# Performance work log

Hardware: AMD Instinct MI355X
Metric: run time of the kernel (lower is better)

The kernel has to match this reference:

```python
import jax, jax.numpy as jnp
import numpy as np

# dims
B, L, IN, H, OUT = 2, 2048, 128, 512, 64
NL, ED, N, DR, K = 2, 1024, 16, 32, 4  # n_layers, d_inner=2*H, d_state, dt_rank=ceil(H/16), d_conv


def setup_inputs() -> dict:
    key = jax.random.key(0)
    ks = jax.random.split(key, 18)
    r = lambda k, s: 0.05 * jax.random.normal(k, s, dtype=jnp.float32)
    return {
        "x": jax.random.normal(ks[0], (B, L, IN), dtype=jnp.float32),
        # LiquidNet proj (in_dim -> hidden -> hidden)
        "p_Wi": r(ks[1], (IN, H)), "p_bi": r(ks[2], (H,)), "p_bh": r(ks[3], (H,)),
        "p_Wo": r(ks[4], (H, H)), "p_bo": r(ks[5], (H,)),
        # Mamba layers (stacked over layer axis)
        "m_norm_w": jnp.ones((NL, H), jnp.float32),
        "m_in_W": r(ks[6], (NL, H, 2 * ED)),
        "m_conv_w": r(ks[7], (NL, ED, K)), "m_conv_b": r(ks[8], (NL, ED)),
        "m_xproj_W": r(ks[9], (NL, ED, DR + 2 * N)),
        "m_dt_W": r(ks[10], (NL, DR, ED)), "m_dt_b": r(ks[11], (NL, ED)),
        "m_A_log": jnp.tile(jnp.log(jnp.arange(1, N + 1, dtype=jnp.float32)), (NL, ED, 1)),
        "m_D": jnp.ones((NL, ED), jnp.float32),
        "m_out_W": r(ks[12], (NL, ED, H)),
        # LiquidNet dense (hidden -> out_dim -> out_dim)
        "d_Wi": r(ks[13], (H, OUT)), "d_bi": r(ks[14], (OUT,)), "d_bh": r(ks[15], (OUT,)),
        "d_Wo": r(ks[16], (OUT, OUT)), "d_bo": r(ks[17], (OUT,)),
    }


def _rmsnorm(x, w, eps=1e-5):
    return x * jax.lax.rsqrt(jnp.mean(x * x, axis=-1, keepdims=True) + eps) * w


def _liquid(x, Wi, bi, bh, Wo, bo):
    # liquid cell with zero initial hidden state: h = tanh(i2h(x) + h2h(0))
    h = jnp.tanh(x @ Wi + bi + bh)
    return h @ Wo + bo


def _causal_conv(x, w, b):
    # x: [B, L, ED]; depthwise causal conv with kernel K
    xt = x.transpose(0, 2, 1)  # [B, ED, L]
    y = jax.lax.conv_general_dilated(xt, w[:, None, :], (1,), [(K - 1, 0)],
                                     dimension_numbers=('NCH', 'OIH', 'NCH'),
                                     feature_group_count=ED)
    return (y + b[None, :, None]).transpose(0, 2, 1)


def _ssm(xc, delta, Bm, Cm, A, D):
    # xc/delta: [B,L,ED]; Bm/Cm: [B,L,N]; A: [ED,N]; D: [ED]
    deltaA = jnp.exp(delta[..., None] * A)                              # [B,L,ED,N]
    deltaBx = delta[..., None] * Bm[:, :, None, :] * xc[..., None]      # [B,L,ED,N]

    def step(h, t):
        dA, dBx, Ct = t
        h = dA * h + dBx
        return h, jnp.einsum('bdn,bn->bd', h, Ct)

    h0 = jnp.zeros((xc.shape[0], ED, N), xc.dtype)
    _, ys = jax.lax.scan(step, h0, (deltaA.transpose(1, 0, 2, 3),
                                    deltaBx.transpose(1, 0, 2, 3),
                                    Cm.transpose(1, 0, 2)))
    return ys.transpose(1, 0, 2) + D * xc


def _mamba_block(x, norm_w, in_W, conv_w, conv_b, xproj_W, dt_W, dt_b, A_log, D, out_W):
    xn = _rmsnorm(x, norm_w)
    xz = xn @ in_W                       # [B,L,2*ED]
    xc, z = jnp.split(xz, 2, axis=-1)
    xc = jax.nn.silu(_causal_conv(xc, conv_w, conv_b))
    dbl = xc @ xproj_W                   # [B,L,DR+2N]
    dt, Bm, Cm = dbl[..., :DR], dbl[..., DR:DR + N], dbl[..., DR + N:]
    delta = jax.nn.softplus(dt @ dt_W + dt_b)
    y = _ssm(xc, delta, Bm, Cm, -jnp.exp(A_log), D)
    y = y * jax.nn.silu(z)
    return y @ out_W


def reference(x, p_Wi, p_bi, p_bh, p_Wo, p_bo,
              m_norm_w, m_in_W, m_conv_w, m_conv_b, m_xproj_W, m_dt_W, m_dt_b,
              m_A_log, m_D, m_out_W,
              d_Wi, d_bi, d_bh, d_Wo, d_bo):
    out = _liquid(x, p_Wi, p_bi, p_bh, p_Wo, p_bo)
    for l in range(NL):  # residual Mamba blocks
        out = out + _mamba_block(out, m_norm_w[l], m_in_W[l], m_conv_w[l], m_conv_b[l],
                                 m_xproj_W[l], m_dt_W[l], m_dt_b[l], m_A_log[l], m_D[l], m_out_W[l])
    out = _liquid(out, d_Wi, d_bi, d_bh, d_Wo, d_bo)
    out = out - jnp.tanh(out)  # Tanhshrink
    return out.reshape(-1)
```

## Files before the change

### kernel.cpp

```cpp
#include <hip/hip_runtime.h>
#include <hip/hip_bf16.h>
#include <cstdint>
#include <cstddef>

#define B_   2
#define L_   2048
#define IN_  128
#define H_   512
#define OUT_ 64
#define NL_  2
#define ED_  1024
#define N_   16
#define DR_  32
#define K_   4

static constexpr int M_TOK = B_ * L_;
static constexpr int SEG   = 64;
static constexpr int TS    = L_ / SEG;

typedef __attribute__((ext_vector_type(8))) short bhalf8;
typedef __attribute__((ext_vector_type(4))) float floatx4;

__device__ __forceinline__ ushort bf16bits(float f)
{
    __hip_bfloat16 h = __float2bfloat16(f);
    return *reinterpret_cast<ushort*>(&h);
}

__device__ __forceinline__ void gld_lds16(const ushort* g, ushort* l)
{
    __builtin_amdgcn_global_load_lds(
        (const __attribute__((address_space(1))) unsigned int*)g,
        (__attribute__((address_space(3))) unsigned int*)l, 16, 0, 0);
}

template<int BM, int BN, int BK, int EPI, bool DUAL>
__global__ __launch_bounds__(256)
void mfma_gemm(const ushort* __restrict__ A, int lda,
               const ushort* Bt, int ldb,
               const ushort* Bt2, float* C2,
               const float* __restrict__ b1, const float* __restrict__ b2,
               float* C, __hip_bfloat16* Cb, int ldc,
               int M, int N, int kc)
{
    __shared__ __align__(16) ushort As[BM * BK];
    __shared__ __align__(16) ushort Bs[BN * BK];

    const int tid  = threadIdx.x;
    const int bm   = blockIdx.x * BM, bn = blockIdx.y * BN;
    int kz = 0, kbeg = 0;
    if (DUAL) {
        if (blockIdx.z) { Bt = Bt2; C = C2; }
    } else {
        kz = blockIdx.z; kbeg = kz * kc;
    }
    const int lane = tid & 63, wave = tid >> 6;
    const int wr = wave >> 1, wc = wave & 1;
    constexpr int WM = BM / 2, WN = BN / 2;
    constexpr int FM = WM / 16, FN = WN / 16;
    const int fr = lane & 15, fg = lane >> 4;

    constexpr int ACH = BM * BK / 512;
    constexpr int BCH = BN * BK / 512;
    constexpr int RPC = 512 / BK;
    constexpr int LPR = BK / 8;
    const int sr = lane / LPR;
    const int sc = (lane % LPR) * 8;

    floatx4 acc[FM][FN] = {};

    for (int k0 = kbeg; k0 < kbeg + kc; k0 += BK) {
        #pragma unroll
        for (int i = 0; i < ACH / 4; ++i) {
            const int ci = wave * (ACH / 4) + i;
            const int r  = ci * RPC + sr;
            gld_lds16(&A[(size_t)(bm + r) * lda + k0 + sc], &As[ci * 512]);
        }
        #pragma unroll
        for (int i = 0; i < BCH / 4; ++i) {
            const int ci = wave * (BCH / 4) + i;
            const int r  = ci * RPC + sr;
            gld_lds16(&Bt[(size_t)(bn + r) * ldb + k0 + sc], &Bs[ci * 512]);
        }
        __syncthreads();
        #pragma unroll
        for (int kk = 0; kk < BK; kk += 32) {
            bhalf8 fa[FM], fb[FN];
            #pragma unroll
            for (int m = 0; m < FM; ++m)
                fa[m] = *reinterpret_cast<const bhalf8*>(
                    &As[(wr * WM + m * 16 + fr) * BK + kk + fg * 8]);
            #pragma unroll
            for (int n = 0; n < FN; ++n)
                fb[n] = *reinterpret_cast<const bhalf8*>(
                    &Bs[(wc * WN + n * 16 + fr) * BK + kk + fg * 8]);
            #pragma unroll
            for (int m = 0; m < FM; ++m)
                #pragma unroll
                for (int n = 0; n < FN; ++n)
                    acc[m][n] = __builtin_amdgcn_mfma_f32_16x16x32_bf16(
                        fa[m], fb[n], acc[m][n], 0, 0, 0);
        }
        __syncthreads();
    }

    #pragma unroll
    for (int m = 0; m < FM; ++m) {
        #pragma unroll
        for (int n = 0; n < FN; ++n) {
            const int row0 = bm + wr * WM + m * 16 + fg * 4;
            const int col  = bn + wc * WN + n * 16 + fr;
            #pragma unroll
            for (int r = 0; r < 4; ++r) {
                float v = acc[m][n][r];
                const int row = row0 + r;
                if (EPI == 0) {
                    C[(size_t)row * ldc + col] = v;
                } else if (EPI == 1) {
                    C[(size_t)row * ldc + col] += v;
                } else if (EPI == 2) {
                    Cb[(size_t)row * ldc + col] =
                        __float2bfloat16(tanhf(v + b1[col] + b2[col]));
                } else if (EPI == 3) {
                    C[(size_t)row * ldc + col] = v + b1[col];
                } else if (EPI == 4) {
                    C[(size_t)kz * M * N + (size_t)row * N + col] = v;
                } else if (EPI == 5) {
                    const float w = v + b1[col];
                    C[(size_t)row * ldc + col] = w - tanhf(w);
                } else if (EPI == 6) {
                    const float w = v + b1[col];
                    C[(size_t)row * ldc + col] =
                        fmaxf(w, 0.0f) + log1pf(expf(-fabsf(w)));
                } else if (EPI == 7) {
                    float* cp = C + (size_t)row * ldc + col;
                    const float w = *cp + v;
                    *cp = w;
                    Cb[(size_t)row * ldc + col] = __float2bfloat16(w);
                }
            }
        }
    }
}

template<int NP, int ACT, bool B1, bool B2, int OUTMODE>
__global__ __launch_bounds__(256)
void reduce_part_k(const float* __restrict__ P, const float* __restrict__ b1,
                   const float* __restrict__ b2, float* __restrict__ Of,
                   __hip_bfloat16* __restrict__ Ob, int MN, int Ncols)
{
    const int i = blockIdx.x * 256 + threadIdx.x;
    float s = 0.0f;
    #pragma unroll
    for (int z = 0; z < NP; ++z) s += P[(size_t)z * MN + i];
    const int col = i & (Ncols - 1);
    if (B1) s += b1[col];
    if (B2) s += b2[col];
    if (ACT == 1) s = tanhf(s);
    if (OUTMODE == 0 || OUTMODE == 2) Of[i] = s;
    if (OUTMODE == 1 || OUTMODE == 2) Ob[i] = __float2bfloat16(s);
}

__device__ __forceinline__ void tr32(float (*t)[33],
                                     const float* __restrict__ W,
                                     __hip_bfloat16* __restrict__ Wt,
                                     int K, int N, int local, int gx, int tid)
{
    const int kx = local % gx, ny = local / gx;
    const int k0 = kx * 32, n0 = ny * 32;
    const int c = tid & 31, r4 = tid >> 5;
    #pragma unroll
    for (int i = 0; i < 4; ++i) {
        const int rr = r4 + i * 8;
        t[rr][c] = W[(size_t)(k0 + rr) * N + n0 + c];
    }
    __syncthreads();
    #pragma unroll
    for (int i = 0; i < 4; ++i) {
        const int rr = r4 + i * 8;
        Wt[(size_t)(n0 + rr) * K + k0 + c] = __float2bfloat16(t[c][rr]);
    }
}

__global__ __launch_bounds__(256)
void prep_k(const float* __restrict__ x, __hip_bfloat16* __restrict__ Xb,
            const float* pWi, __hip_bfloat16* TpWi,
            const float* pWo, __hip_bfloat16* TpWo,
            const float* inW, __hip_bfloat16* TinW0, __hip_bfloat16* TinW1,
            const float* xpW, __hip_bfloat16* TxpW0, __hip_bfloat16* TxpW1,
            const float* outW, __hip_bfloat16* ToutW0, __hip_bfloat16* ToutW1,
            const float* dWi, __hip_bfloat16* TdWi,
            const float* dtW, __hip_bfloat16* TdtW0, __hip_bfloat16* TdtW1,
            const float* dWo, __hip_bfloat16* TdWo)
{
    __shared__ float t[32][33];
    const int tid = threadIdx.x;
    int r = blockIdx.x;

    if (r < 512) {
        const int i = (r * 256 + tid) * 4;
        const float4 v = *reinterpret_cast<const float4*>(&x[i]);
        ushort4 u;
        u.x = bf16bits(v.x); u.y = bf16bits(v.y);
        u.z = bf16bits(v.z); u.w = bf16bits(v.w);
        *reinterpret_cast<ushort4*>(&Xb[i]) = u;
        return;
    }
    r -= 512;
    if (r < 64)   { tr32(t, pWi, TpWi, IN_, H_, r, 4, tid); return; }   r -= 64;
    if (r < 256)  { tr32(t, pWo, TpWo, H_, H_, r, 16, tid); return; }   r -= 256;
    if (r < 1024) { tr32(t, inW, TinW0, H_, 2 * ED_, r, 16, tid); return; } r -= 1024;
    if (r < 1024) { tr32(t, inW + (size_t)H_ * 2 * ED_, TinW1, H_, 2 * ED_, r, 16, tid); return; } r -= 1024;
    if (r < 64)   { tr32(t, xpW, TxpW0, ED_, 64, r, 32, tid); return; } r -= 64;
    if (r < 64)   { tr32(t, xpW + (size_t)ED_ * 64, TxpW1, ED_, 64, r, 32, tid); return; } r -= 64;
    if (r < 512)  { tr32(t, outW, ToutW0, ED_, H_, r, 32, tid); return; } r -= 512;
    if (r < 512)  { tr32(t, outW + (size_t)ED_ * H_, ToutW1, ED_, H_, r, 32, tid); return; } r -= 512;
    if (r < 32)   { tr32(t, dWi, TdWi, H_, OUT_, r, 16, tid); return; } r -= 32;
    if (r < 32)   { tr32(t, dtW, TdtW0, DR_, ED_, r, 1, tid); return; } r -= 32;
    if (r < 32)   { tr32(t, dtW + DR_ * ED_, TdtW1, DR_, ED_, r, 1, tid); return; } r -= 32;
    tr32(t, dWo, TdWo, OUT_, OUT_, r, 2, tid);
}
static constexpr int PREP_BLOCKS = 512 + 64 + 256 + 1024 + 1024 + 64 + 64 + 512 + 512 + 32 + 32 + 32 + 4;

__global__ __launch_bounds__(256)
void rmsnorm_k(const float* __restrict__ x, const float* __restrict__ w,
               __hip_bfloat16* __restrict__ o)
{
    const int row = blockIdx.x;
    const int tid = threadIdx.x;
    const float* xr = x + (size_t)row * H_;
    float v0 = xr[tid], v1 = xr[tid + 256];
    float s = v0 * v0 + v1 * v1;
    #pragma unroll
    for (int off = 32; off > 0; off >>= 1) s += __shfl_down(s, off, 64);
    __shared__ float ps[4];
    __shared__ float scale_s;
    const int wave = tid >> 6, lane = tid & 63;
    if (lane == 0) ps[wave] = s;
    __syncthreads();
    if (tid == 0) {
        float tot = ps[0] + ps[1] + ps[2] + ps[3];
        scale_s = rsqrtf(tot * (1.0f / H_) + 1e-5f);
    }
    __syncthreads();
    const float sc = scale_s;
    o[(size_t)row * H_ + tid]       = __float2bfloat16(v0 * sc * w[tid]);
    o[(size_t)row * H_ + tid + 256] = __float2bfloat16(v1 * sc * w[tid + 256]);
}

__global__ __launch_bounds__(256)
void conv_silu_k(const float* __restrict__ xcr, const float* __restrict__ cw,
                 const float* __restrict__ cb, float* __restrict__ xc,
                 __hip_bfloat16* __restrict__ xcb)
{
    const int idx = blockIdx.x * 256 + threadIdx.x;
    const int d4 = (idx & (ED_ / 4 - 1)) * 4;
    const int t  = (idx >> 8) & (L_ - 1);
    const int b  = idx >> 19;
    const size_t base = (size_t)(b * L_ + t) * ED_ + d4;

    float4 x0 = *reinterpret_cast<const float4*>(&xcr[base]);
    float4 x1 = {}, x2 = {}, x3 = {};
    if (t >= 1) x1 = *reinterpret_cast<const float4*>(&xcr[base - 1 * ED_]);
    if (t >= 2) x2 = *reinterpret_cast<const float4*>(&xcr[base - 2 * ED_]);
    if (t >= 3) x3 = *reinterpret_cast<const float4*>(&xcr[base - 3 * ED_]);
    const float4 bias = *reinterpret_cast<const float4*>(&cb[d4]);

    float4 out;
    ushort4 outb;
    #pragma unroll
    for (int j = 0; j < 4; ++j) {
        const float4 w = *reinterpret_cast<const float4*>(&cw[(d4 + j) * 4]);
        float acc = (&bias.x)[j];
        acc += w.w * (&x0.x)[j];
        acc += w.z * (&x1.x)[j];
        acc += w.y * (&x2.x)[j];
        acc += w.x * (&x3.x)[j];
        const float s = acc / (1.0f + __expf(-acc));
        (&out.x)[j] = s;
        (&outb.x)[j] = bf16bits(s);
    }
    *reinterpret_cast<float4*>(&xc[base]) = out;
    *reinterpret_cast<ushort4*>(&xcb[base]) = outb;
}

template<bool P3>
__global__ __launch_bounds__(256)
void ssm_scan_k(const float* __restrict__ delta,
                const float* __restrict__ xc,
                const float* __restrict__ dbl,
                const float* __restrict__ zbuf,
                const float* __restrict__ A_log,
                const float* __restrict__ Dv,
                float* __restrict__ hend, float* __restrict__ pprod,
                const float* __restrict__ hinit,
                __hip_bfloat16* __restrict__ ybuf)
{
    __shared__ float sdl[TS][64];
    __shared__ float sxc[TS][64];
    __shared__ float bc[TS][32];
    const int bx   = blockIdx.x;
    const int seg  = bx & (SEG - 1);
    const int dblk = (bx >> 6) & 15;
    const int b    = bx >> 10;
    const int tid  = threadIdx.x;
    const int dl   = tid >> 2;
    const int ng   = tid & 3;
    const int d    = dblk * 64 + dl;
    const int dbase = dblk * 64;
    const size_t row0 = (size_t)(b * L_ + seg * TS);

    #pragma unroll
    for (int e = 0; e < 8; ++e) {
        const int lin = tid + e * 256;
        sdl[lin >> 6][lin & 63] = delta[(row0 + (lin >> 6)) * ED_ + dbase + (lin & 63)];
    }
    #pragma unroll
    for (int e = 0; e < 8; ++e) {
        const int lin = tid + e * 256;
        sxc[lin >> 6][lin & 63] = xc[(row0 + (lin >> 6)) * ED_ + dbase + (lin & 63)];
    }
    #pragma unroll
    for (int e = 0; e < 4; ++e) {
        const int lin = tid + e * 256;
        bc[lin >> 5][lin & 31] = dbl[(row0 + (lin >> 5)) * 64 + 32 + (lin & 31)];
    }

    float Av[4];
    #pragma unroll
    for (int i = 0; i < 4; ++i) Av[i] = -expf(A_log[d * N_ + ng * 4 + i]);

    float h[4], P[4];
    if (P3) {
        #pragma unroll
        for (int i = 0; i < 4; ++i)
            h[i] = hinit[((size_t)(b * SEG + seg) * N_ + ng * 4 + i) * ED_ + d];
    } else {
        #pragma unroll
        for (int i = 0; i < 4; ++i) { h[i] = 0.0f; P[i] = 1.0f; }
    }
    const float Dd = P3 ? Dv[d] : 0.0f;
    __syncthreads();

    #pragma unroll
    for (int t = 0; t < TS; ++t) {
        const float dvt = sdl[t][dl];
        const float xvt = sxc[t][dl];
        const float dx  = dvt * xvt;
        float ysum = 0.0f;
        #pragma unroll
        for (int i = 0; i < 4; ++i) {
            const float dA = __expf(dvt * Av[i]);
            h[i] = fmaf(dA, h[i], dx * bc[t][ng * 4 + i]);
            if (!P3) P[i] *= dA;
            else     ysum = fmaf(h[i], bc[t][16 + ng * 4 + i], ysum);
        }
        if (P3) {
            float y2 = ysum + __shfl_xor(ysum, 1, 64);
            float y4 = y2 + __shfl_xor(y2, 2, 64);
            if (ng == 0) {
                const float zv = zbuf[(row0 + t) * ED_ + d];
                const float sz = zv / (1.0f + __expf(-zv));
                ybuf[(row0 + t) * ED_ + d] =
                    __float2bfloat16((y4 + Dd * xvt) * sz);
            }
        }
    }

    if (!P3) {
        #pragma unroll
        for (int i = 0; i < 4; ++i) {
            const size_t o = ((size_t)(b * SEG + seg) * N_ + ng * 4 + i) * ED_ + d;
            hend[o]  = h[i];
            pprod[o] = P[i];
        }
    }
}

__global__ __launch_bounds__(256)
void ssm_combine_k(const float* __restrict__ hend, const float* __restrict__ pprod,
                   float* __restrict__ hinit)
{
    const int gid = blockIdx.x * 256 + threadIdx.x;
    const int d = gid & (ED_ - 1);
    const int n = (gid >> 10) & (N_ - 1);
    const int b = gid >> 14;
    size_t o = ((size_t)(b * SEG) * N_ + n) * ED_ + d;
    const size_t stride = (size_t)N_ * ED_;
    float h = 0.0f;
    #pragma unroll 8
    for (int s = 0; s < SEG; ++s) {
        hinit[o] = h;
        h = fmaf(pprod[o], h, hend[o]);
        o += stride;
    }
}

extern "C" void kernel_launch(void* const* d_in, const int* in_sizes, int n_in,
                              void* d_out, int out_size, void* d_ws, size_t ws_size,
                              hipStream_t stream)
{
    const float* x      = (const float*)d_in[0];
    const float* p_Wi   = (const float*)d_in[1];
    const float* p_bi   = (const float*)d_in[2];
    const float* p_bh   = (const float*)d_in[3];
    const float* p_Wo   = (const float*)d_in[4];
    const float* p_bo   = (const float*)d_in[5];
    const float* m_norm = (const float*)d_in[6];
    const float* m_inW  = (const float*)d_in[7];
    const float* m_cw   = (const float*)d_in[8];
    const float* m_cb   = (const float*)d_in[9];
    const float* m_xpW  = (const float*)d_in[10];
    const float* m_dtW  = (const float*)d_in[11];
    const float* m_dtb  = (const float*)d_in[12];
    const float* m_Alog = (const float*)d_in[13];
    const float* m_D    = (const float*)d_in[14];
    const float* m_outW = (const float*)d_in[15];
    const float* d_Wi   = (const float*)d_in[16];
    const float* d_bi   = (const float*)d_in[17];
    const float* d_bh   = (const float*)d_in[18];
    const float* d_Wo   = (const float*)d_in[19];
    const float* d_bo   = (const float*)d_in[20];
    float* out_f = (float*)d_out;
    float* ws = (float*)d_ws;

    float* OUT   = ws;
    float* XCR   = ws + 2097152;
    float* Z     = ws + 6291456;
    float* XC    = ws + 10485760;
    float* DBL   = ws + 14680064;
    float* DELTA = ws + 14942208;
    float* HINIT = ws + 19136512;
    float* BF    = ws + 21233664;
    float* WT    = ws + 23330816;
    float* DBLF  = ws + 25184256;

    float* HEND   = XCR;
    float* PPROD  = XCR + 2097152;
    float* CPARTX = DELTA;
    float* CPART2 = XCR;
    __hip_bfloat16* Xb   = (__hip_bfloat16*)BF;
    __hip_bfloat16* H1b  = (__hip_bfloat16*)(BF + 262144);
    __hip_bfloat16* XNb  = (__hip_bfloat16*)BF;
    __hip_bfloat16* XCb  = (__hip_bfloat16*)BF;
    __hip_bfloat16* YB   = (__hip_bfloat16*)BF;
    __hip_bfloat16* H2b  = (__hip_bfloat16*)BF;
    __hip_bfloat16* OUTb = (__hip_bfloat16*)XC;
    __hip_bfloat16* DBLb = (__hip_bfloat16*)DBLF;

    __hip_bfloat16* WTu     = (__hip_bfloat16*)WT;
    __hip_bfloat16* T_pWi   = WTu;
    __hip_bfloat16* T_pWo   = WTu + 65536;
    __hip_bfloat16* T_inW0  = WTu + 327680;
    __hip_bfloat16* T_inW1  = WTu + 1376256;
    __hip_bfloat16* T_xpW0  = WTu + 2424832;
    __hip_bfloat16* T_xpW1  = WTu + 2490368;
    __hip_bfloat16* T_outW0 = WTu + 2555904;
    __hip_bfloat16* T_outW1 = WTu + 3080192;
    __hip_bfloat16* T_dWi   = WTu + 3604480;
    __hip_bfloat16* T_dtW0  = WTu + 3637248;
    __hip_bfloat16* T_dtW1  = WTu + 3670016;
    __hip_bfloat16* T_dWo   = WTu + 3702784;

    const dim3 blk(256);

    prep_k<<<dim3(PREP_BLOCKS), blk, 0, stream>>>(
        x, Xb, p_Wi, T_pWi, p_Wo, T_pWo, m_inW, T_inW0, T_inW1,
        m_xpW, T_xpW0, T_xpW1, m_outW, T_outW0, T_outW1,
        d_Wi, T_dWi, m_dtW, T_dtW0, T_dtW1, d_Wo, T_dWo);

    mfma_gemm<128, 64, 64, 2, false><<<dim3(32, 8), blk, 0, stream>>>(
        (const ushort*)Xb, IN_, (const ushort*)T_pWi, IN_, nullptr, nullptr,
        p_bi, p_bh, nullptr, H1b, H_, M_TOK, H_, IN_);
    mfma_gemm<128, 64, 64, 3, false><<<dim3(32, 8), blk, 0, stream>>>(
        (const ushort*)H1b, H_, (const ushort*)T_pWo, H_, nullptr, nullptr,
        p_bo, nullptr, OUT, nullptr, H_, M_TOK, H_, H_);

    for (int l = 0; l < NL_; ++l) {
        const float* nw   = m_norm + l * H_;
        const float* cw   = m_cw   + l * ED_ * K_;
        const float* cb   = m_cb   + l * ED_;
        const float* dtb  = m_dtb  + l * ED_;
        const float* Alog = m_Alog + l * ED_ * N_;
        const float* Dv   = m_D    + l * ED_;
        const __hip_bfloat16* TinW  = l ? T_inW1  : T_inW0;
        const __hip_bfloat16* TxpW  = l ? T_xpW1  : T_xpW0;
        const __hip_bfloat16* ToutW = l ? T_outW1 : T_outW0;
        const __hip_bfloat16* TdtW  = l ? T_dtW1  : T_dtW0;

        rmsnorm_k<<<dim3(M_TOK), blk, 0, stream>>>(OUT, nw, XNb);
        mfma_gemm<128, 128, 64, 0, true><<<dim3(32, 8, 2), blk, 0, stream>>>(
            (const ushort*)XNb, H_, (const ushort*)TinW, H_,
            (const ushort*)(TinW + (size_t)ED_ * H_), Z,
            nullptr, nullptr, XCR, nullptr, ED_, M_TOK, ED_, H_);
        conv_silu_k<<<dim3(M_TOK * ED_ / 4 / 256), blk, 0, stream>>>(XCR, cw, cb, XC, XCb);
        mfma_gemm<128, 64, 64, 4, false><<<dim3(32, 1, 8), blk, 0, stream>>>(
            (const ushort*)XCb, ED_, (const ushort*)TxpW, ED_, nullptr, nullptr,
            nullptr, nullptr, CPARTX, nullptr, 64, M_TOK, 64, ED_ / 8);
        reduce_part_k<8, 0, false, false, 2><<<dim3(1024), blk, 0, stream>>>(
            CPARTX, nullptr, nullptr, DBL, DBLb, M_TOK * 64, 64);
        mfma_gemm<128, 64, 32, 6, false><<<dim3(32, 16), blk, 0, stream>>>(
            (const ushort*)DBLb, 64, (const ushort*)TdtW, DR_, nullptr, nullptr,
            dtb, nullptr, DELTA, nullptr, ED_, M_TOK, ED_, DR_);
        ssm_scan_k<false><<<dim3(2048), blk, 0, stream>>>(
            DELTA, XC, DBL, nullptr, Alog, nullptr, HEND, PPROD, nullptr, nullptr);
        ssm_combine_k<<<dim3(128), blk, 0, stream>>>(HEND, PPROD, HINIT);
        ssm_scan_k<true><<<dim3(2048), blk, 0, stream>>>(
            DELTA, XC, DBL, Z, Alog, Dv, nullptr, nullptr, HINIT, YB);
        if (l == 0) {
            mfma_gemm<128, 64, 64, 1, false><<<dim3(32, 8), blk, 0, stream>>>(
                (const ushort*)YB, ED_, (const ushort*)ToutW, ED_, nullptr, nullptr,
                nullptr, nullptr, OUT, nullptr, H_, M_TOK, H_, ED_);
        } else {
            mfma_gemm<128, 64, 64, 7, false><<<dim3(32, 8), blk, 0, stream>>>(
                (const ushort*)YB, ED_, (const ushort*)ToutW, ED_, nullptr, nullptr,
                nullptr, nullptr, OUT, OUTb, H_, M_TOK, H_, ED_);
        }
    }

    mfma_gemm<128, 64, 64, 4, false><<<dim3(32, 1, 8), blk, 0, stream>>>(
        (const ushort*)OUTb, H_, (const ushort*)T_dWi, H_, nullptr, nullptr,
        nullptr, nullptr, CPART2, nullptr, 64, M_TOK, 64, H_ / 8);
    reduce_part_k<8, 1, true, true, 1><<<dim3(1024), blk, 0, stream>>>(
        CPART2, d_bi, d_bh, nullptr, H2b, M_TOK * 64, 64);
    mfma_gemm<128, 64, 64, 5, false><<<dim3(32, 1), blk, 0, stream>>>(
        (const ushort*)H2b, OUT_, (const ushort*)T_dWo, OUT_, nullptr, nullptr,
        d_bo, nullptr, out_f, nullptr, OUT_, M_TOK, OUT_, OUT_);
}
```

Before: 342.5 us.

## Fuse dt projection, softplus and conv recompute into SSM scan kernels

Removes the separate delta GEMM (dt_proj plus softplus) and the fp32 XC buffer. Each scan block now recomputes the causal conv plus SiLU from the raw XCR values and computes delta from dbl and the dt weights in shared memory. This cuts global traffic for the fp32 delta and xc tensors (each written once and read twice) and drops one launch per layer. The cost is redundant FP32 compute in both scan passes and larger shared memory per block, which could lower occupancy.

After: 408.7 us. 19.3% more time.

```diff
diff --git a/kernel.cpp b/kernel.cpp
--- a/kernel.cpp
+++ b/kernel.cpp
@@ -128,10 +128,6 @@
                 } else if (EPI == 5) {
                     const float w = v + b1[col];
                     C[(size_t)row * ldc + col] = w - tanhf(w);
-                } else if (EPI == 6) {
-                    const float w = v + b1[col];
-                    C[(size_t)row * ldc + col] =
-                        fmaxf(w, 0.0f) + log1pf(expf(-fabsf(w)));
                 } else if (EPI == 7) {
                     float* cp = C + (size_t)row * ldc + col;
                     const float w = *cp + v;
@@ -190,7 +186,6 @@
             const float* xpW, __hip_bfloat16* TxpW0, __hip_bfloat16* TxpW1,
             const float* outW, __hip_bfloat16* ToutW0, __hip_bfloat16* ToutW1,
             const float* dWi, __hip_bfloat16* TdWi,
-            const float* dtW, __hip_bfloat16* TdtW0, __hip_bfloat16* TdtW1,
             const float* dWo, __hip_bfloat16* TdWo)
 {
     __shared__ float t[32][33];
@@ -216,11 +211,9 @@
     if (r < 512)  { tr32(t, outW, ToutW0, ED_, H_, r, 32, tid); return; } r -= 512;
     if (r < 512)  { tr32(t, outW + (size_t)ED_ * H_, ToutW1, ED_, H_, r, 32, tid); return; } r -= 512;
     if (r < 32)   { tr32(t, dWi, TdWi, H_, OUT_, r, 16, tid); return; } r -= 32;
-    if (r < 32)   { tr32(t, dtW, TdtW0, DR_, ED_, r, 1, tid); return; } r -= 32;
-    if (r < 32)   { tr32(t, dtW + DR_ * ED_, TdtW1, DR_, ED_, r, 1, tid); return; } r -= 32;
     tr32(t, dWo, TdWo, OUT_, OUT_, r, 2, tid);
 }
-static constexpr int PREP_BLOCKS = 512 + 64 + 256 + 1024 + 1024 + 64 + 64 + 512 + 512 + 32 + 32 + 32 + 4;
+static constexpr int PREP_BLOCKS = 512 + 64 + 256 + 1024 + 1024 + 64 + 64 + 512 + 512 + 32 + 4;
 
 __global__ __launch_bounds__(256)
 void rmsnorm_k(const float* __restrict__ x, const float* __restrict__ w,
@@ -250,8 +243,7 @@
 
 __global__ __launch_bounds__(256)
 void conv_silu_k(const float* __restrict__ xcr, const float* __restrict__ cw,
-                 const float* __restrict__ cb, float* __restrict__ xc,
-                 __hip_bfloat16* __restrict__ xcb)
+                 const float* __restrict__ cb, __hip_bfloat16* __restrict__ xcb)
 {
     const int idx = blockIdx.x * 256 + threadIdx.x;
     const int d4 = (idx & (ED_ / 4 - 1)) * 4;
@@ -266,7 +258,6 @@
     if (t >= 3) x3 = *reinterpret_cast<const float4*>(&xcr[base - 3 * ED_]);
     const float4 bias = *reinterpret_cast<const float4*>(&cb[d4]);
 
-    float4 out;
     ushort4 outb;
     #pragma unroll
     for (int j = 0; j < 4; ++j) {
@@ -277,18 +268,19 @@
         acc += w.y * (&x2.x)[j];
         acc += w.x * (&x3.x)[j];
         const float s = acc / (1.0f + __expf(-acc));
-        (&out.x)[j] = s;
         (&outb.x)[j] = bf16bits(s);
     }
-    *reinterpret_cast<float4*>(&xc[base]) = out;
     *reinterpret_cast<ushort4*>(&xcb[base]) = outb;
 }
 
 template<bool P3>
 __global__ __launch_bounds__(256)
-void ssm_scan_k(const float* __restrict__ delta,
-                const float* __restrict__ xc,
+void ssm_scan_k(const float* __restrict__ xcr,
                 const float* __restrict__ dbl,
+                const float* __restrict__ dtw,
+                const float* __restrict__ dtb,
+                const float* __restrict__ cw,
+                const float* __restrict__ cb,
                 const float* __restrict__ zbuf,
                 const float* __restrict__ A_log,
                 const float* __restrict__ Dv,
@@ -296,35 +288,73 @@
                 const float* __restrict__ hinit,
                 __hip_bfloat16* __restrict__ ybuf)
 {
-    __shared__ float sdl[TS][64];
-    __shared__ float sxc[TS][64];
-    __shared__ float bc[TS][32];
+    __shared__ float sdbl[TS][64];
+    __shared__ float sdtw[32][64];
+    __shared__ float sxc [TS][64];
+    __shared__ float sxcr[36][64];
+
     const int bx   = blockIdx.x;
     const int seg  = bx & (SEG - 1);
     const int dblk = (bx >> 6) & 15;
     const int b    = bx >> 10;
     const int tid  = threadIdx.x;
-    const int dl   = tid >> 2;
-    const int ng   = tid & 3;
-    const int d    = dblk * 64 + dl;
     const int dbase = dblk * 64;
-    const size_t row0 = (size_t)(b * L_ + seg * TS);
+    const int t0   = seg * TS;
+    const size_t row0 = (size_t)(b * L_ + t0);
+    const int dls = tid & 63;
 
     #pragma unroll
     for (int e = 0; e < 8; ++e) {
+        const int t = (tid + e * 256) >> 6;
+        sdbl[t][dls] = dbl[(row0 + t) * 64 + dls];
+    }
+    #pragma unroll
+    for (int e = 0; e < 8; ++e) {
+        const int k = (tid + e * 256) >> 6;
+        sdtw[k][dls] = dtw[k * ED_ + dbase + dls];
+    }
+    #pragma unroll
+    for (int e = 0; e < 9; ++e) {
         const int lin = tid + e * 256;
-        sdl[lin >> 6][lin & 63] = delta[(row0 + (lin >> 6)) * ED_ + dbase + (lin & 63)];
-    }
-    #pragma unroll
-    for (int e = 0; e < 8; ++e) {
-        const int lin = tid + e * 256;
-        sxc[lin >> 6][lin & 63] = xc[(row0 + (lin >> 6)) * ED_ + dbase + (lin & 63)];
-    }
-    #pragma unroll
-    for (int e = 0; e < 4; ++e) {
-        const int lin = tid + e * 256;
-        bc[lin >> 5][lin & 31] = dbl[(row0 + (lin >> 5)) * 64 + 32 + (lin & 31)];
-    }
+        if (lin < 35 * 64) {
+            const int rr = lin >> 6;
+            const int gt = t0 - 3 + rr;
+            sxcr[rr][dls] = (gt >= 0)
+                ? xcr[((size_t)(b * L_ + gt)) * ED_ + dbase + dls] : 0.0f;
+        }
+    }
+    __syncthreads();
+
+    {
+        const float4 wv = *reinterpret_cast<const float4*>(&cw[(dbase + dls) * 4]);
+        const float cbv = cb[dbase + dls];
+        #pragma unroll
+        for (int e = 0; e < 8; ++e) {
+            const int t = (tid + e * 256) >> 6;
+            float a = cbv + wv.x * sxcr[t][dls] + wv.y * sxcr[t + 1][dls]
+                          + wv.z * sxcr[t + 2][dls] + wv.w * sxcr[t + 3][dls];
+            sxc[t][dls] = a / (1.0f + __expf(-a));
+        }
+    }
+    __syncthreads();
+
+    {
+        const float dtbv = dtb[dbase + dls];
+        #pragma unroll
+        for (int e = 0; e < 8; ++e) {
+            const int t = (tid + e * 256) >> 6;
+            float s = dtbv;
+            #pragma unroll
+            for (int k = 0; k < 32; ++k)
+                s = fmaf(sdbl[t][k], sdtw[k][dls], s);
+            sxcr[t][dls] = fmaxf(s, 0.0f) + log1pf(expf(-fabsf(s)));
+        }
+    }
+    __syncthreads();
+
+    const int dl = tid >> 2;
+    const int ng = tid & 3;
+    const int d  = dbase + dl;
 
     float Av[4];
     #pragma unroll
@@ -340,20 +370,19 @@
         for (int i = 0; i < 4; ++i) { h[i] = 0.0f; P[i] = 1.0f; }
     }
     const float Dd = P3 ? Dv[d] : 0.0f;
-    __syncthreads();
 
     #pragma unroll
     for (int t = 0; t < TS; ++t) {
-        const float dvt = sdl[t][dl];
+        const float dvt = sxcr[t][dl];
         const float xvt = sxc[t][dl];
         const float dx  = dvt * xvt;
         float ysum = 0.0f;
         #pragma unroll
         for (int i = 0; i < 4; ++i) {
             const float dA = __expf(dvt * Av[i]);
-            h[i] = fmaf(dA, h[i], dx * bc[t][ng * 4 + i]);
+            h[i] = fmaf(dA, h[i], dx * sdbl[t][32 + ng * 4 + i]);
             if (!P3) P[i] *= dA;
-            else     ysum = fmaf(h[i], bc[t][16 + ng * 4 + i], ysum);
+            else     ysum = fmaf(h[i], sdbl[t][48 + ng * 4 + i], ysum);
         }
         if (P3) {
             float y2 = ysum + __shfl_xor(ysum, 1, 64);
@@ -427,17 +456,15 @@
     float* OUT   = ws;
     float* XCR   = ws + 2097152;
     float* Z     = ws + 6291456;
-    float* XC    = ws + 10485760;
-    float* DBL   = ws + 14680064;
-    float* DELTA = ws + 14942208;
-    float* HINIT = ws + 19136512;
-    float* BF    = ws + 21233664;
-    float* WT    = ws + 23330816;
-    float* DBLF  = ws + 25184256;
-
-    float* HEND   = XCR;
-    float* PPROD  = XCR + 2097152;
-    float* CPARTX = DELTA;
+    float* HEND  = ws + 10485760;
+    float* PPROD = ws + 12582912;
+    float* HINIT = ws + 14680064;
+    float* PART  = ws + 16777216;
+    float* BF    = ws + 18874368;
+    float* WT    = ws + 20971520;
+    float* DBL   = ws + 22792192;
+
+    float* CPARTX = PART;
     float* CPART2 = XCR;
     __hip_bfloat16* Xb   = (__hip_bfloat16*)BF;
     __hip_bfloat16* H1b  = (__hip_bfloat16*)(BF + 262144);
@@ -445,8 +472,7 @@
     __hip_bfloat16* XCb  = (__hip_bfloat16*)BF;
     __hip_bfloat16* YB   = (__hip_bfloat16*)BF;
     __hip_bfloat16* H2b  = (__hip_bfloat16*)BF;
-    __hip_bfloat16* OUTb = (__hip_bfloat16*)XC;
-    __hip_bfloat16* DBLb = (__hip_bfloat16*)DBLF;
+    __hip_bfloat16* OUTb = (__hip_bfloat16*)PART;
 
     __hip_bfloat16* WTu     = (__hip_bfloat16*)WT;
     __hip_bfloat16* T_pWi   = WTu;
@@ -458,16 +484,14 @@
     __hip_bfloat16* T_outW0 = WTu + 2555904;
     __hip_bfloat16* T_outW1 = WTu + 3080192;
     __hip_bfloat16* T_dWi   = WTu + 3604480;
-    __hip_bfloat16* T_dtW0  = WTu + 3637248;
-    __hip_bfloat16* T_dtW1  = WTu + 3670016;
-    __hip_bfloat16* T_dWo   = WTu + 3702784;
+    __hip_bfloat16* T_dWo   = WTu + 3637248;
 
     const dim3 blk(256);
 
     prep_k<<<dim3(PREP_BLOCKS), blk, 0, stream>>>(
         x, Xb, p_Wi, T_pWi, p_Wo, T_pWo, m_inW, T_inW0, T_inW1,
         m_xpW, T_xpW0, T_xpW1, m_outW, T_outW0, T_outW1,
-        d_Wi, T_dWi, m_dtW, T_dtW0, T_dtW1, d_Wo, T_dWo);
+        d_Wi, T_dWi, d_Wo, T_dWo);
 
     mfma_gemm<128, 64, 64, 2, false><<<dim3(32, 8), blk, 0, stream>>>(
         (const ushort*)Xb, IN_, (const ushort*)T_pWi, IN_, nullptr, nullptr,
@@ -480,33 +504,32 @@
         const float* nw   = m_norm + l * H_;
         const float* cw   = m_cw   + l * ED_ * K_;
         const float* cb   = m_cb   + l * ED_;
+        const float* dtw  = m_dtW  + l * DR_ * ED_;
         const float* dtb  = m_dtb  + l * ED_;
         const float* Alog = m_Alog + l * ED_ * N_;
         const float* Dv   = m_D    + l * ED_;
         const __hip_bfloat16* TinW  = l ? T_inW1  : T_inW0;
         const __hip_bfloat16* TxpW  = l ? T_xpW1  : T_xpW0;
         const __hip_bfloat16* ToutW = l ? T_outW1 : T_outW0;
-        const __hip_bfloat16* TdtW  = l ? T_dtW1  : T_dtW0;
 
         rmsnorm_k<<<dim3(M_TOK), blk, 0, stream>>>(OUT, nw, XNb);
         mfma_gemm<128, 128, 64, 0, true><<<dim3(32, 8, 2), blk, 0, stream>>>(
             (const ushort*)XNb, H_, (const ushort*)TinW, H_,
             (const ushort*)(TinW + (size_t)ED_ * H_), Z,
             nullptr, nullptr, XCR, nullptr, ED_, M_TOK, ED_, H_);
-        conv_silu_k<<<dim3(M_TOK * ED_ / 4 / 256), blk, 0, stream>>>(XCR, cw, cb, XC, XCb);
+        conv_silu_k<<<dim3(M_TOK * ED_ / 4 / 256), blk, 0, stream>>>(XCR, cw, cb, XCb);
         mfma_gemm<128, 64, 64, 4, false><<<dim3(32, 1, 8), blk, 0, stream>>>(
             (const ushort*)XCb, ED_, (const ushort*)TxpW, ED_, nullptr, nullptr,
             nullptr, nullptr, CPARTX, nullptr, 64, M_TOK, 64, ED_ / 8);
-        reduce_part_k<8, 0, false, false, 2><<<dim3(1024), blk, 0, stream>>>(
-            CPARTX, nullptr, nullptr, DBL, DBLb, M_TOK * 64, 64);
-        mfma_gemm<128, 64, 32, 6, false><<<dim3(32, 16), blk, 0, stream>>>(
-            (const ushort*)DBLb, 64, (const ushort*)TdtW, DR_, nullptr, nullptr,
-            dtb, nullptr, DELTA, nullptr, ED_, M_TOK, ED_, DR_);
+        reduce_part_k<8, 0, false, false, 0><<<dim3(1024), blk, 0, stream>>>(
+            CPARTX, nullptr, nullptr, DBL, nullptr, M_TOK * 64, 64);
         ssm_scan_k<false><<<dim3(2048), blk, 0, stream>>>(
-            DELTA, XC, DBL, nullptr, Alog, nullptr, HEND, PPROD, nullptr, nullptr);
+            XCR, DBL, dtw, dtb, cw, cb, nullptr, Alog, nullptr,
+            HEND, PPROD, nullptr, nullptr);
         ssm_combine_k<<<dim3(128), blk, 0, stream>>>(HEND, PPROD, HINIT);
         ssm_scan_k<true><<<dim3(2048), blk, 0, stream>>>(
-            DELTA, XC, DBL, Z, Alog, Dv, nullptr, nullptr, HINIT, YB);
+            XCR, DBL, dtw, dtb, cw, cb, Z, Alog, Dv,
+            nullptr, nullptr, HINIT, YB);
         if (l == 0) {
             mfma_gemm<128, 64, 64, 1, false><<<dim3(32, 8), blk, 0, stream>>>(
                 (const ushort*)YB, ED_, (const ushort*)ToutW, ED_, nullptr, nullptr,
```

## Fuse causal conv+SiLU into x-proj GEMM and SSM scans, drop XC buffer

Applied to the files above, without the earlier changes.

Removes the standalone conv_silu kernel. The depthwise causal conv and SiLU are now recomputed from the raw projection both in the A-tile load of a new x-proj GEMM and in the shared-memory staging of both SSM scan passes. The first scan pass now derives the segment decay product in closed form as exp(A*sum(delta)) rather than multiplying per step. The aim is to avoid writing and re-reading the fp32 and bf16 conv outputs. The cost is redundant conv arithmetic, halo reloads, and a reshuffled workspace layout.

Result: faster. 327.7 us (-4.3%).

```diff
diff --git a/kernel.cpp b/kernel.cpp
--- a/kernel.cpp
+++ b/kernel.cpp
@@ -143,6 +143,109 @@
     }
 }
 
+__global__ __launch_bounds__(256)
+void xproj_gemm(const float* __restrict__ xcr,
+                const float* __restrict__ cw, const float* __restrict__ cb,
+                const ushort* __restrict__ Bt,
+                float* __restrict__ Cpart)
+{
+    __shared__ __align__(16) ushort As[128 * 64];
+    __shared__ __align__(16) ushort Bs[64 * 64];
+
+    const int tid = threadIdx.x;
+    const int bm  = blockIdx.x * 128;
+    const int kz  = blockIdx.z;
+    const int lane = tid & 63, wave = tid >> 6;
+    const int wr = wave >> 1, wc = wave & 1;
+    const int fr = lane & 15, fg = lane >> 4;
+    const int tseq0 = bm & (L_ - 1);
+
+    const int col8 = (tid & 7) * 8;
+    const int rq   = tid >> 3;
+    const int sr   = lane / 8, sc2 = (lane & 7) * 8;
+
+    floatx4 acc[4][2] = {};
+
+    #pragma unroll
+    for (int ks = 0; ks < 2; ++ks) {
+        const int k0 = kz * 128 + ks * 64;
+
+        float4 wv[8]; float cbv[8];
+        #pragma unroll
+        for (int j = 0; j < 8; ++j) {
+            wv[j]  = *reinterpret_cast<const float4*>(&cw[(k0 + col8 + j) * 4]);
+            cbv[j] = cb[k0 + col8 + j];
+        }
+        float xr[7][8];
+        #pragma unroll
+        for (int ii = 0; ii < 7; ++ii) {
+            const int tok = bm + rq * 4 - 3 + ii;
+            const int tokc = tok < 0 ? 0 : tok;
+            const float4 a = *reinterpret_cast<const float4*>(
+                &xcr[(size_t)tokc * ED_ + k0 + col8]);
+            const float4 b = *reinterpret_cast<const float4*>(
+                &xcr[(size_t)tokc * ED_ + k0 + col8 + 4]);
+            xr[ii][0]=a.x; xr[ii][1]=a.y; xr[ii][2]=a.z; xr[ii][3]=a.w;
+            xr[ii][4]=b.x; xr[ii][5]=b.y; xr[ii][6]=b.z; xr[ii][7]=b.w;
+        }
+        #pragma unroll
+        for (int rr = 0; rr < 4; ++rr) {
+            const int trow = tseq0 + rq * 4 + rr;
+            __align__(16) ushort ob[8];
+            #pragma unroll
+            for (int j = 0; j < 8; ++j) {
+                float a = cbv[j] + wv[j].w * xr[rr + 3][j];
+                if (trow >= 1) a += wv[j].z * xr[rr + 2][j];
+                if (trow >= 2) a += wv[j].y * xr[rr + 1][j];
+                if (trow >= 3) a += wv[j].x * xr[rr + 0][j];
+                const float s = a / (1.0f + __expf(-a));
+                ob[j] = bf16bits(s);
+            }
+            *reinterpret_cast<uint4*>(&As[(rq * 4 + rr) * 64 + col8]) =
+                *reinterpret_cast<const uint4*>(ob);
+        }
+        #pragma unroll
+        for (int i = 0; i < 2; ++i) {
+            const int ci = wave * 2 + i;
+            const int r  = ci * 8 + sr;
+            gld_lds16(&Bt[(size_t)r * ED_ + k0 + sc2], &Bs[ci * 512]);
+        }
+        __syncthreads();
+        #pragma unroll
+        for (int kk = 0; kk < 64; kk += 32) {
+            bhalf8 fa[4], fb[2];
+            #pragma unroll
+            for (int m = 0; m < 4; ++m)
+                fa[m] = *reinterpret_cast<const bhalf8*>(
+                    &As[(wr * 64 + m * 16 + fr) * 64 + kk + fg * 8]);
+            #pragma unroll
+            for (int n = 0; n < 2; ++n)
+                fb[n] = *reinterpret_cast<const bhalf8*>(
+                    &Bs[(wc * 32 + n * 16 + fr) * 64 + kk + fg * 8]);
+            #pragma unroll
+            for (int m = 0; m < 4; ++m)
+                #pragma unroll
+                for (int n = 0; n < 2; ++n)
+                    acc[m][n] = __builtin_amdgcn_mfma_f32_16x16x32_bf16(
+                        fa[m], fb[n], acc[m][n], 0, 0, 0);
+        }
+        __syncthreads();
+    }
+
+    #pragma unroll
+    for (int m = 0; m < 4; ++m) {
+        #pragma unroll
+        for (int n = 0; n < 2; ++n) {
+            const int row0 = bm + wr * 64 + m * 16 + fg * 4;
+            const int col  = wc * 32 + n * 16 + fr;
+            #pragma unroll
+            for (int r = 0; r < 4; ++r)
+                Cpart[(size_t)kz * M_TOK * 64 + (size_t)(row0 + r) * 64 + col] =
+                    acc[m][n][r];
+        }
+    }
+}
+
 template<int NP, int ACT, bool B1, bool B2, int OUTMODE>
 __global__ __launch_bounds__(256)
 void reduce_part_k(const float* __restrict__ P, const float* __restrict__ b1,
@@ -248,47 +351,12 @@
     o[(size_t)row * H_ + tid + 256] = __float2bfloat16(v1 * sc * w[tid + 256]);
 }
 
-__global__ __launch_bounds__(256)
-void conv_silu_k(const float* __restrict__ xcr, const float* __restrict__ cw,
-                 const float* __restrict__ cb, float* __restrict__ xc,
-                 __hip_bfloat16* __restrict__ xcb)
-{
-    const int idx = blockIdx.x * 256 + threadIdx.x;
-    const int d4 = (idx & (ED_ / 4 - 1)) * 4;
-    const int t  = (idx >> 8) & (L_ - 1);
-    const int b  = idx >> 19;
-    const size_t base = (size_t)(b * L_ + t) * ED_ + d4;
-
-    float4 x0 = *reinterpret_cast<const float4*>(&xcr[base]);
-    float4 x1 = {}, x2 = {}, x3 = {};
-    if (t >= 1) x1 = *reinterpret_cast<const float4*>(&xcr[base - 1 * ED_]);
-    if (t >= 2) x2 = *reinterpret_cast<const float4*>(&xcr[base - 2 * ED_]);
-    if (t >= 3) x3 = *reinterpret_cast<const float4*>(&xcr[base - 3 * ED_]);
-    const float4 bias = *reinterpret_cast<const float4*>(&cb[d4]);
-
-    float4 out;
-    ushort4 outb;
-    #pragma unroll
-    for (int j = 0; j < 4; ++j) {
-        const float4 w = *reinterpret_cast<const float4*>(&cw[(d4 + j) * 4]);
-        float acc = (&bias.x)[j];
-        acc += w.w * (&x0.x)[j];
-        acc += w.z * (&x1.x)[j];
-        acc += w.y * (&x2.x)[j];
-        acc += w.x * (&x3.x)[j];
-        const float s = acc / (1.0f + __expf(-acc));
-        (&out.x)[j] = s;
-        (&outb.x)[j] = bf16bits(s);
-    }
-    *reinterpret_cast<float4*>(&xc[base]) = out;
-    *reinterpret_cast<ushort4*>(&xcb[base]) = outb;
-}
-
 template<bool P3>
 __global__ __launch_bounds__(256)
 void ssm_scan_k(const float* __restrict__ delta,
-                const float* __restrict__ xc,
+                const float* __restrict__ xcr,
                 const float* __restrict__ dbl,
+                const float* __restrict__ cw, const float* __restrict__ cb,
                 const float* __restrict__ zbuf,
                 const float* __restrict__ A_log,
                 const float* __restrict__ Dv,
@@ -299,61 +367,80 @@
     __shared__ float sdl[TS][64];
     __shared__ float sxc[TS][64];
     __shared__ float bc[TS][32];
+
     const int bx   = blockIdx.x;
     const int seg  = bx & (SEG - 1);
     const int dblk = (bx >> 6) & 15;
     const int b    = bx >> 10;
     const int tid  = threadIdx.x;
-    const int dl   = tid >> 2;
-    const int ng   = tid & 3;
-    const int d    = dblk * 64 + dl;
     const int dbase = dblk * 64;
-    const size_t row0 = (size_t)(b * L_ + seg * TS);
+    const int t0   = seg * TS;
+    const size_t row0 = (size_t)(b * L_ + t0);
+    const int dls = tid & 63;
 
     #pragma unroll
     for (int e = 0; e < 8; ++e) {
-        const int lin = tid + e * 256;
-        sdl[lin >> 6][lin & 63] = delta[(row0 + (lin >> 6)) * ED_ + dbase + (lin & 63)];
-    }
-    #pragma unroll
-    for (int e = 0; e < 8; ++e) {
-        const int lin = tid + e * 256;
-        sxc[lin >> 6][lin & 63] = xc[(row0 + (lin >> 6)) * ED_ + dbase + (lin & 63)];
+        const int t = (tid >> 6) + e * 4;
+        sdl[t][dls] = delta[(row0 + t) * ED_ + dbase + dls];
+    }
+    {
+        const int tg = tid >> 6;
+        const int tb = tg * 8;
+        float xr[11];
+        #pragma unroll
+        for (int ii = 0; ii < 11; ++ii) {
+            const int gt = t0 + tb - 3 + ii;
+            xr[ii] = (gt >= 0)
+                ? xcr[((size_t)(b * L_) + gt) * ED_ + dbase + dls] : 0.0f;
+        }
+        const float4 w = *reinterpret_cast<const float4*>(&cw[(dbase + dls) * 4]);
+        const float cbv = cb[dbase + dls];
+        #pragma unroll
+        for (int k = 0; k < 8; ++k) {
+            const float a = cbv + w.x * xr[k] + w.y * xr[k + 1]
+                          + w.z * xr[k + 2] + w.w * xr[k + 3];
+            sxc[tb + k][dls] = a / (1.0f + __expf(-a));
+        }
     }
     #pragma unroll
     for (int e = 0; e < 4; ++e) {
         const int lin = tid + e * 256;
         bc[lin >> 5][lin & 31] = dbl[(row0 + (lin >> 5)) * 64 + 32 + (lin & 31)];
     }
+    __syncthreads();
+
+    const int dl = tid >> 2;
+    const int ng = tid & 3;
+    const int d  = dbase + dl;
 
     float Av[4];
     #pragma unroll
     for (int i = 0; i < 4; ++i) Av[i] = -expf(A_log[d * N_ + ng * 4 + i]);
 
-    float h[4], P[4];
+    float h[4];
+    float S = 0.0f;
     if (P3) {
         #pragma unroll
         for (int i = 0; i < 4; ++i)
             h[i] = hinit[((size_t)(b * SEG + seg) * N_ + ng * 4 + i) * ED_ + d];
     } else {
         #pragma unroll
-        for (int i = 0; i < 4; ++i) { h[i] = 0.0f; P[i] = 1.0f; }
+        for (int i = 0; i < 4; ++i) h[i] = 0.0f;
     }
     const float Dd = P3 ? Dv[d] : 0.0f;
-    __syncthreads();
 
     #pragma unroll
     for (int t = 0; t < TS; ++t) {
         const float dvt = sdl[t][dl];
         const float xvt = sxc[t][dl];
         const float dx  = dvt * xvt;
+        if (!P3) S += dvt;
         float ysum = 0.0f;
         #pragma unroll
         for (int i = 0; i < 4; ++i) {
             const float dA = __expf(dvt * Av[i]);
             h[i] = fmaf(dA, h[i], dx * bc[t][ng * 4 + i]);
-            if (!P3) P[i] *= dA;
-            else     ysum = fmaf(h[i], bc[t][16 + ng * 4 + i], ysum);
+            if (P3) ysum = fmaf(h[i], bc[t][16 + ng * 4 + i], ysum);
         }
         if (P3) {
             float y2 = ysum + __shfl_xor(ysum, 1, 64);
@@ -372,7 +459,7 @@
         for (int i = 0; i < 4; ++i) {
             const size_t o = ((size_t)(b * SEG + seg) * N_ + ng * 4 + i) * ED_ + d;
             hend[o]  = h[i];
-            pprod[o] = P[i];
+            pprod[o] = __expf(Av[i] * S);
         }
     }
 }
@@ -427,25 +514,23 @@
     float* OUT   = ws;
     float* XCR   = ws + 2097152;
     float* Z     = ws + 6291456;
-    float* XC    = ws + 10485760;
-    float* DBL   = ws + 14680064;
-    float* DELTA = ws + 14942208;
-    float* HINIT = ws + 19136512;
-    float* BF    = ws + 21233664;
-    float* WT    = ws + 23330816;
+    float* DELTA = ws + 10485760;
+    float* HEND  = ws + 14680064;
+    float* PPROD = ws + 16777216;
+    float* HINIT = ws + 18874368;
+    float* BF    = ws + 20971520;
+    float* WT    = ws + 23068672;
+    float* DBL   = ws + 24922112;
     float* DBLF  = ws + 25184256;
 
-    float* HEND   = XCR;
-    float* PPROD  = XCR + 2097152;
-    float* CPARTX = DELTA;
+    float* CPARTX = HEND;
     float* CPART2 = XCR;
     __hip_bfloat16* Xb   = (__hip_bfloat16*)BF;
     __hip_bfloat16* H1b  = (__hip_bfloat16*)(BF + 262144);
     __hip_bfloat16* XNb  = (__hip_bfloat16*)BF;
-    __hip_bfloat16* XCb  = (__hip_bfloat16*)BF;
     __hip_bfloat16* YB   = (__hip_bfloat16*)BF;
-    __hip_bfloat16* H2b  = (__hip_bfloat16*)BF;
-    __hip_bfloat16* OUTb = (__hip_bfloat16*)XC;
+    __hip_bfloat16* H2b  = (__hip_bfloat16*)DBL;
+    __hip_bfloat16* OUTb = (__hip_bfloat16*)PPROD;
     __hip_bfloat16* DBLb = (__hip_bfloat16*)DBLF;
 
     __hip_bfloat16* WTu     = (__hip_bfloat16*)WT;
@@ -493,20 +578,20 @@
             (const ushort*)XNb, H_, (const ushort*)TinW, H_,
             (const ushort*)(TinW + (size_t)ED_ * H_), Z,
             nullptr, nullptr, XCR, nullptr, ED_, M_TOK, ED_, H_);
-        conv_silu_k<<<dim3(M_TOK * ED_ / 4 / 256), blk, 0, stream>>>(XCR, cw, cb, XC, XCb);
-        mfma_gemm<128, 64, 64, 4, false><<<dim3(32, 1, 8), blk, 0, stream>>>(
-            (const ushort*)XCb, ED_, (const ushort*)TxpW, ED_, nullptr, nullptr,
-            nullptr, nullptr, CPARTX, nullptr, 64, M_TOK, 64, ED_ / 8);
+        xproj_gemm<<<dim3(32, 1, 8), blk, 0, stream>>>(
+            XCR, cw, cb, (const ushort*)TxpW, CPARTX);
         reduce_part_k<8, 0, false, false, 2><<<dim3(1024), blk, 0, stream>>>(
             CPARTX, nullptr, nullptr, DBL, DBLb, M_TOK * 64, 64);
         mfma_gemm<128, 64, 32, 6, false><<<dim3(32, 16), blk, 0, stream>>>(
             (const ushort*)DBLb, 64, (const ushort*)TdtW, DR_, nullptr, nullptr,
             dtb, nullptr, DELTA, nullptr, ED_, M_TOK, ED_, DR_);
         ssm_scan_k<false><<<dim3(2048), blk, 0, stream>>>(
-            DELTA, XC, DBL, nullptr, Alog, nullptr, HEND, PPROD, nullptr, nullptr);
+            DELTA, XCR, DBL, cw, cb, nullptr, Alog, nullptr,
+            HEND, PPROD, nullptr, nullptr);
         ssm_combine_k<<<dim3(128), blk, 0, stream>>>(HEND, PPROD, HINIT);
         ssm_scan_k<true><<<dim3(2048), blk, 0, stream>>>(
-            DELTA, XC, DBL, Z, Alog, Dv, nullptr, nullptr, HINIT, YB);
+            DELTA, XCR, DBL, cw, cb, Z, Alog, Dv,
+            nullptr, nullptr, HINIT, YB);
         if (l == 0) {
             mfma_gemm<128, 64, 64, 1, false><<<dim3(32, 8), blk, 0, stream>>>(
                 (const ushort*)YB, ED_, (const ushort*)ToutW, ED_, nullptr, nullptr,
```
